# Optimization experiments

Measured on AMD Instinct MI355X. Metric: run time of the kernel, lower is better.

The kernel has to match this reference:

```python
import jax, jax.numpy as jnp
import numpy as np

N = 50000
E = 1600000
EP = 500000
D_IN, D_EMB = 64, 32


def setup_inputs() -> dict:
    key = jax.random.key(0)
    ks = jax.random.split(key, 12)
    return {
        "x": jax.random.normal(ks[0], (N, D_IN), dtype=jnp.float32),
        "W1": jax.random.normal(ks[1], (D_IN, D_EMB), dtype=jnp.float32) * (1.0 / np.sqrt(D_IN)),
        "b1": jnp.zeros((D_EMB,), dtype=jnp.float32),
        "W2": jax.random.normal(ks[2], (D_EMB, 2 * D_EMB), dtype=jnp.float32) * (1.0 / np.sqrt(D_EMB)),
        "b2": jnp.zeros((2 * D_EMB,), dtype=jnp.float32),
        "eps": jax.random.normal(ks[3], (N, D_EMB), dtype=jnp.float32),
        "edge_src": jax.random.randint(ks[4], (E,), 0, N, dtype=jnp.int32),
        "edge_dst": jax.random.randint(ks[5], (E,), 0, N, dtype=jnp.int32),
        "pos_src": jax.random.randint(ks[6], (EP,), 0, N, dtype=jnp.int32),
        "pos_dst": jax.random.randint(ks[7], (EP,), 0, N, dtype=jnp.int32),
        "neg_src": jax.random.randint(ks[8], (EP,), 0, N, dtype=jnp.int32),
        "neg_dst": jax.random.randint(ks[9], (EP,), 0, N, dtype=jnp.int32),
    }


def _degree_norms(src, dst, n):
    ones = jnp.ones(src.shape, dtype=jnp.float32)
    out_deg = jax.ops.segment_sum(ones, src, num_segments=n)
    in_deg = jax.ops.segment_sum(ones, dst, num_segments=n)
    # DGL GraphConv norm='both': clamp degrees to >=1, pow(-0.5)
    return jnp.clip(out_deg, 1.0) ** -0.5, jnp.clip(in_deg, 1.0) ** -0.5


def _graph_conv(h, src, dst, norm_src, norm_dst, W, b, n):
    # rst = D_dst^{-1/2} A D_src^{-1/2} h W + b
    msg = (h * norm_src[:, None])[src]                       # [E, d] gather
    agg = jax.ops.segment_sum(msg, dst, num_segments=n)      # [N, d] scatter-add
    return (agg * norm_dst[:, None]) @ W + b


def _dot_predict(z, u, v):
    # u_dot_v: per-edge inner product of endpoint embeddings
    return jnp.sum(z[u] * z[v], axis=-1)


def reference(x, W1, b1, W2, b2, eps, edge_src, edge_dst,
              pos_src, pos_dst, neg_src, neg_dst):
    n = x.shape[0]
    ns, nd = _degree_norms(edge_src, edge_dst, n)
    h = _graph_conv(x, edge_src, edge_dst, ns, nd, W1, b1, n)
    h = jax.nn.relu(h)  # dropout = identity (eval mode)
    h = _graph_conv(h, edge_src, edge_dst, ns, nd, W2, b2, n)
    mu, log_var = jnp.split(h, 2, axis=-1)
    sigma = jnp.exp(log_var / 2.0)
    z = mu + sigma * eps
    pos = _dot_predict(z, pos_src, pos_dst)
    neg = _dot_predict(z, neg_src, neg_dst)
    return pos, neg, mu, sigma
```

## Files before the change

kernel.cpp:

```cpp
#include <hip/hip_runtime.h>
#include <math.h>

#define NN  50000
#define NE  1600000
#define NEP 500000
#define DIN 64
#define DE  32

#define BKT_SH 7
#define NB     391
#define S1B    250
#define CHK    6400
#define HB     128
#define HCHK   12500
#define HWRD   12500
#define XWB    3125

__device__ __forceinline__ unsigned f2b(float f) {
    unsigned u = __float_as_uint(f);
    return (u + 0x7FFFu + ((u >> 16) & 1u)) >> 16;
}
__device__ __forceinline__ unsigned pack2(float a, float b) {
    return f2b(a) | (f2b(b) << 16);
}
__device__ __forceinline__ float blo(unsigned u) { return __uint_as_float(u << 16); }
__device__ __forceinline__ float bhi(unsigned u) { return __uint_as_float(u & 0xFFFF0000u); }

__global__ __launch_bounds__(256) void k_h1s1(const int* __restrict__ src,
                                              const int* __restrict__ dst,
                                              unsigned* __restrict__ partial,
                                              int* __restrict__ T) {
    __shared__ unsigned h[HWRD];
    int t = threadIdx.x;
    if (blockIdx.x < HB) {
        for (int i = t; i < HWRD; i += 256) h[i] = 0;
        __syncthreads();
        int beg = blockIdx.x * HCHK;
        for (int i = beg + t; i < beg + HCHK; i += 256) {
            int s = src[i];
            atomicAdd(&h[s >> 2], 1u << ((s & 3) * 8));
        }
        __syncthreads();
        unsigned* p = partial + (size_t)blockIdx.x * HWRD;
        for (int i = t; i < HWRD; i += 256) p[i] = h[i];
    } else {
        int b = blockIdx.x - HB;
        int* cd = (int*)h;
        for (int i = t; i < NB; i += 256) cd[i] = 0;
        __syncthreads();
        int beg = b * CHK;
        for (int i = beg + t; i < beg + CHK; i += 256)
            atomicAdd(&cd[dst[i] >> BKT_SH], 1);
        __syncthreads();
        for (int i = t; i < NB; i += 256) T[b * NB + i] = cd[i];
    }
}

__global__ __launch_bounds__(512) void k_s2h(const int* __restrict__ T,
                                             int* __restrict__ Base,
                                             int* __restrict__ BS,
                                             const unsigned* __restrict__ partial,
                                             int* __restrict__ degs) {
    int t = threadIdx.x;
    if (blockIdx.x == 0) {
        __shared__ int tot[512];
        int run = 0;
        if (t < NB) {
            for (int b = 0; b < S1B; b++) {
                Base[b * NB + t] = run;
                run += T[b * NB + t];
            }
        }
        tot[t] = (t < NB) ? run : 0;
        __syncthreads();
        for (int off = 1; off < 512; off <<= 1) {
            int v = (t >= off) ? tot[t - off] : 0;
            __syncthreads();
            tot[t] += v;
            __syncthreads();
        }
        if (t < NB) BS[t] = (t == 0) ? 0 : tot[t - 1];
        if (t == 0) BS[NB] = NE;
    } else {
        int w = (blockIdx.x - 1) * 512 + t;
        if (w < HWRD) {
            int c0 = 0, c1 = 0, c2 = 0, c3 = 0;
            for (int b = 0; b < HB; b++) {
                unsigned v = partial[(size_t)b * HWRD + w];
                c0 += (int)(v & 0xFFu);
                c1 += (int)((v >> 8) & 0xFFu);
                c2 += (int)((v >> 16) & 0xFFu);
                c3 += (int)(v >> 24);
            }
            ((int4*)degs)[w] = make_int4(c0, c1, c2, c3);
        }
    }
}

__global__ __launch_bounds__(512) void k_s3(const int* __restrict__ src,
                                            const int* __restrict__ dst,
                                            const int* __restrict__ T,
                                            const int* __restrict__ Base,
                                            const int* __restrict__ BS,
                                            unsigned* __restrict__ tmp) {
    __shared__ int scn[512];
    __shared__ int delta[NB];
    __shared__ int cur[NB];
    __shared__ unsigned buf[CHK];
    int t = threadIdx.x;
    int beg = blockIdx.x * CHK;
    scn[t] = (t < NB) ? T[blockIdx.x * NB + t] : 0;
    __syncthreads();
    for (int off = 1; off < 512; off <<= 1) {
        int v = (t >= off) ? scn[t - off] : 0;
        __syncthreads();
        scn[t] += v;
        __syncthreads();
    }
    if (t < NB) {
        int ls = (t == 0) ? 0 : scn[t - 1];
        cur[t] = ls;
        delta[t] = Base[blockIdx.x * NB + t] + BS[t] - ls;
    }
    __syncthreads();
    for (int i = t; i < CHK; i += 512) {
        int d = dst[beg + i];
        int s = src[beg + i];
        int lp = atomicAdd(&cur[d >> BKT_SH], 1);
        buf[lp] = (unsigned)s | ((unsigned)d << 16);
    }
    __syncthreads();
    for (int i = t; i < CHK; i += 512) {
        unsigned e = buf[i];
        tmp[delta[e >> (16 + BKT_SH)] + i] = e;
    }
}

__global__ __launch_bounds__(256) void k_s4x(const unsigned* __restrict__ tmp,
                                             const int* __restrict__ BS,
                                             int* __restrict__ csr,
                                             int* __restrict__ rowptr,
                                             const float* __restrict__ x,
                                             const float* __restrict__ W1,
                                             const int* __restrict__ degs,
                                             unsigned* __restrict__ xw1b) {
    __shared__ float sW[DIN * DE];
    int t = threadIdx.x;
    if (blockIdx.x < NB) {
        int* cnt = (int*)sW;
        int* scn = cnt + 128;
        int* cur = cnt + 256;
        int p = blockIdx.x;
        int ebeg = BS[p], eend = BS[p + 1];
        int ne = eend - ebeg;
        if (t < 128) cnt[t] = 0;
        __syncthreads();
        for (int i = t; i < ne; i += 256)
            atomicAdd(&cnt[(tmp[ebeg + i] >> 16) & 127], 1);
        __syncthreads();
        if (t < 128) scn[t] = cnt[t];
        __syncthreads();
        for (int off = 1; off < 128; off <<= 1) {
            int v = 0;
            if (t < 128 && t >= off) v = scn[t - off];
            __syncthreads();
            if (t < 128) scn[t] += v;
            __syncthreads();
        }
        if (t < 128) {
            int ex = (t == 0) ? 0 : scn[t - 1];
            cur[t] = ex;
            int node = (p << BKT_SH) + t;
            if (node < NN) rowptr[node] = ebeg + ex;
        }
        if (p == NB - 1 && t == 0) rowptr[NN] = NE;
        __syncthreads();
        for (int i = t; i < ne; i += 256) {
            unsigned e = tmp[ebeg + i];
            int lp = atomicAdd(&cur[(e >> 16) & 127], 1);
            csr[ebeg + lp] = (int)(e & 0xFFFFu);
        }
    } else {
        for (int i = t; i < DIN * DE; i += 256) sW[i] = W1[i];
        __syncthreads();
        int r  = (blockIdx.x - NB) * 16 + (t >> 4);
        int tc = t & 15;
        const float* xr = x + (size_t)r * DIN;
        float a0 = 0.f, a1 = 0.f;
#pragma unroll
        for (int k = 0; k < DIN; k++) {
            float v = xr[k];
            a0 += v * sW[k * DE + 2 * tc];
            a1 += v * sW[k * DE + 2 * tc + 1];
        }
        float ns = rsqrtf(fmaxf((float)degs[r], 1.0f));
        xw1b[r * 16 + tc] = pack2(a0 * ns, a1 * ns);
    }
}

__device__ __forceinline__ void acc8(float* a, uint4 w) {
    a[0] += blo(w.x); a[1] += bhi(w.x);
    a[2] += blo(w.y); a[3] += bhi(w.y);
    a[4] += blo(w.z); a[5] += bhi(w.z);
    a[6] += blo(w.w); a[7] += bhi(w.w);
}

__device__ __forceinline__ void gather_row(const int* __restrict__ csr,
                                           const uint4* __restrict__ msg,
                                           int beg, int end, int l, float* a) {
    int idx = beg;
    for (; idx + 8 <= end; idx += 8) {
        int s0 = csr[idx],     s1 = csr[idx + 1], s2 = csr[idx + 2], s3 = csr[idx + 3];
        int s4 = csr[idx + 4], s5 = csr[idx + 5], s6 = csr[idx + 6], s7 = csr[idx + 7];
        uint4 w0 = msg[s0 * 4 + l];
        uint4 w1 = msg[s1 * 4 + l];
        uint4 w2 = msg[s2 * 4 + l];
        uint4 w3 = msg[s3 * 4 + l];
        uint4 w4 = msg[s4 * 4 + l];
        uint4 w5 = msg[s5 * 4 + l];
        uint4 w6 = msg[s6 * 4 + l];
        uint4 w7 = msg[s7 * 4 + l];
        acc8(a, w0); acc8(a, w1); acc8(a, w2); acc8(a, w3);
        acc8(a, w4); acc8(a, w5); acc8(a, w6); acc8(a, w7);
    }
    for (; idx + 4 <= end; idx += 4) {
        int s0 = csr[idx], s1 = csr[idx + 1], s2 = csr[idx + 2], s3 = csr[idx + 3];
        uint4 w0 = msg[s0 * 4 + l];
        uint4 w1 = msg[s1 * 4 + l];
        uint4 w2 = msg[s2 * 4 + l];
        uint4 w3 = msg[s3 * 4 + l];
        acc8(a, w0); acc8(a, w1); acc8(a, w2); acc8(a, w3);
    }
    for (; idx < end; idx++) {
        uint4 w = msg[csr[idx] * 4 + l];
        acc8(a, w);
    }
}

__global__ __launch_bounds__(256) void k_g1(const int* __restrict__ rowptr,
                                            const int* __restrict__ csr,
                                            const uint4* __restrict__ msg,
                                            const int* __restrict__ degs,
                                            const float* __restrict__ b1,
                                            uint4* __restrict__ out) {
    int t = blockIdx.x * 256 + threadIdx.x;
    int r = t >> 2;
    int l = t & 3;
    if (r >= NN) return;
    int beg = rowptr[r];
    int end = rowptr[r + 1];
    float a[8] = {0, 0, 0, 0, 0, 0, 0, 0};
    gather_row(csr, msg, beg, end, l, a);
    float scd = rsqrtf(fmaxf((float)(end - beg), 1.0f));
    float scs = rsqrtf(fmaxf((float)degs[r], 1.0f));
    const float4* b14 = (const float4*)b1;
    float4 bb0 = b14[2 * l], bb1 = b14[2 * l + 1];
    float o0 = fmaxf(scd * a[0] + bb0.x, 0.f) * scs;
    float o1 = fmaxf(scd * a[1] + bb0.y, 0.f) * scs;
    float o2 = fmaxf(scd * a[2] + bb0.z, 0.f) * scs;
    float o3 = fmaxf(scd * a[3] + bb0.w, 0.f) * scs;
    float o4 = fmaxf(scd * a[4] + bb1.x, 0.f) * scs;
    float o5 = fmaxf(scd * a[5] + bb1.y, 0.f) * scs;
    float o6 = fmaxf(scd * a[6] + bb1.z, 0.f) * scs;
    float o7 = fmaxf(scd * a[7] + bb1.w, 0.f) * scs;
    out[r * 4 + l] = make_uint4(pack2(o0, o1), pack2(o2, o3), pack2(o4, o5), pack2(o6, o7));
}

__global__ __launch_bounds__(256) void k_g2f(const int* __restrict__ rowptr,
                                             const int* __restrict__ csr,
                                             const uint4* __restrict__ msg,
                                             const float* __restrict__ W2,
                                             const float* __restrict__ b2,
                                             const float* __restrict__ eps,
                                             float* __restrict__ mu,
                                             float* __restrict__ sigma,
                                             unsigned* __restrict__ zb) {
    __shared__ float sW[DE * 64];
    __shared__ float sb[64];
    int t = threadIdx.x;
    for (int i = t; i < DE * 64; i += 256) sW[i] = W2[i];
    if (t < 64) sb[t] = b2[t];
    __syncthreads();
    int g = blockIdx.x * 256 + t;
    int r = g >> 2;
    int l = g & 3;
    if (r >= NN) return;
    int beg = rowptr[r];
    int end = rowptr[r + 1];
    float a[8] = {0, 0, 0, 0, 0, 0, 0, 0};
    gather_row(csr, msg, beg, end, l, a);
    float scd = rsqrtf(fmaxf((float)(end - beg), 1.0f));
#pragma unroll
    for (int k = 0; k < 8; k++) a[k] *= scd;
    int cbase = 16 * l;
    float o3[16];
#pragma unroll
    for (int j = 0; j < 16; j++) o3[j] = sb[cbase + j];
#pragma unroll
    for (int d = 0; d < 4; d++) {
        int kb = 8 * (l ^ d);
#pragma unroll
        for (int k = 0; k < 8; k++) {
            float av = (d == 0) ? a[k] : __shfl_xor(a[k], d);
            const float* wrow = sW + (kb + k) * 64 + cbase;
#pragma unroll
            for (int j = 0; j < 16; j++) o3[j] += av * wrow[j];
        }
    }
    if (l < 2) {
        float4* mp = (float4*)(mu + (size_t)r * DE + 16 * l);
        mp[0] = make_float4(o3[0],  o3[1],  o3[2],  o3[3]);
        mp[1] = make_float4(o3[4],  o3[5],  o3[6],  o3[7]);
        mp[2] = make_float4(o3[8],  o3[9],  o3[10], o3[11]);
        mp[3] = make_float4(o3[12], o3[13], o3[14], o3[15]);
    }
    float muv[16];
#pragma unroll
    for (int j = 0; j < 16; j++) muv[j] = __shfl_xor(o3[j], 2);
    if (l >= 2) {
        int cc = 16 * (l - 2);
        const float4* ep = (const float4*)(eps + (size_t)r * DE + cc);
        float4 e0 = ep[0], e1 = ep[1], e2 = ep[2], e3 = ep[3];
        float ev[16] = {e0.x, e0.y, e0.z, e0.w, e1.x, e1.y, e1.z, e1.w,
                        e2.x, e2.y, e2.z, e2.w, e3.x, e3.y, e3.z, e3.w};
        float sgv[16], zv[16];
#pragma unroll
        for (int j = 0; j < 16; j++) {
            sgv[j] = expf(0.5f * o3[j]);
            zv[j]  = muv[j] + sgv[j] * ev[j];
        }
        float4* sp = (float4*)(sigma + (size_t)r * DE + cc);
        sp[0] = make_float4(sgv[0],  sgv[1],  sgv[2],  sgv[3]);
        sp[1] = make_float4(sgv[4],  sgv[5],  sgv[6],  sgv[7]);
        sp[2] = make_float4(sgv[8],  sgv[9],  sgv[10], sgv[11]);
        sp[3] = make_float4(sgv[12], sgv[13], sgv[14], sgv[15]);
        uint4* zp = (uint4*)(zb + (size_t)r * 16 + (l - 2) * 8);
        zp[0] = make_uint4(pack2(zv[0], zv[1]), pack2(zv[2], zv[3]),
                           pack2(zv[4], zv[5]), pack2(zv[6], zv[7]));
        zp[1] = make_uint4(pack2(zv[8],  zv[9]),  pack2(zv[10], zv[11]),
                           pack2(zv[12], zv[13]), pack2(zv[14], zv[15]));
    }
}

__global__ __launch_bounds__(256) void k_dot2(const uint4* __restrict__ zb4,
                                              const int* __restrict__ pu,
                                              const int* __restrict__ pv,
                                              const int* __restrict__ nu,
                                              const int* __restrict__ nv,
                                              float* __restrict__ out) {
    int t = blockIdx.x * 256 + threadIdx.x;
    int e = t >> 2;
    int l = t & 3;
    if (e < 2 * NEP) {
        int ee = (e < NEP) ? e : e - NEP;
        const int* uu = (e < NEP) ? pu : nu;
        const int* vv = (e < NEP) ? pv : nv;
        int a = uu[ee];
        int b = vv[ee];
        uint4 za = zb4[a * 4 + l];
        uint4 zc = zb4[b * 4 + l];
        float s = blo(za.x) * blo(zc.x) + bhi(za.x) * bhi(zc.x)
                + blo(za.y) * blo(zc.y) + bhi(za.y) * bhi(zc.y)
                + blo(za.z) * blo(zc.z) + bhi(za.z) * bhi(zc.z)
                + blo(za.w) * blo(zc.w) + bhi(za.w) * bhi(zc.w);
        s += __shfl_xor(s, 1);
        s += __shfl_xor(s, 2);
        if (l == 0) out[e] = s;
    }
}

extern "C" void kernel_launch(void* const* d_in, const int* in_sizes, int n_in,
                              void* d_out, int out_size, void* d_ws, size_t ws_size,
                              hipStream_t stream) {
    const float* x    = (const float*)d_in[0];
    const float* W1   = (const float*)d_in[1];
    const float* b1   = (const float*)d_in[2];
    const float* W2   = (const float*)d_in[3];
    const float* b2   = (const float*)d_in[4];
    const float* eps  = (const float*)d_in[5];
    const int*   esrc = (const int*)d_in[6];
    const int*   edst = (const int*)d_in[7];
    const int*   psrc = (const int*)d_in[8];
    const int*   pdst = (const int*)d_in[9];
    const int*   gsrc = (const int*)d_in[10];
    const int*   gdst = (const int*)d_in[11];

    float* out = (float*)d_out;
    float* pos = out;
    float* mu  = out + 2 * NEP;
    float* sg  = out + 2 * NEP + NN * DE;

    int* wi = (int*)d_ws;
    int*      rowptr  = wi;
    int*      T       = wi + 50001;
    int*      Base    = wi + 147751;
    int*      BS      = wi + 245501;
    int*      degs    = wi + 245896;
    int*      csr     = wi + 295896;
    unsigned* partial = (unsigned*)(wi + 1895896);
    unsigned* tmp     = (unsigned*)(wi + 3495896);
    unsigned* P0      = (unsigned*)(wi + 5095896);
    unsigned* P1      = P0 + 16 * NN;

    k_h1s1<<<HB + S1B, 256, 0, stream>>>(esrc, edst, partial, T);
    k_s2h <<<1 + (HWRD + 511) / 512, 512, 0, stream>>>(T, Base, BS, partial, degs);
    k_s3  <<<S1B, 512, 0, stream>>>(esrc, edst, T, Base, BS, tmp);
    k_s4x <<<NB + XWB, 256, 0, stream>>>(tmp, BS, csr, rowptr, x, W1, degs, P0);
    k_g1  <<<(NN * 4 + 255) / 256, 256, 0, stream>>>(rowptr, csr, (const uint4*)P0, degs, b1, (uint4*)P1);
    k_g2f <<<(NN * 4 + 255) / 256, 256, 0, stream>>>(rowptr, csr, (const uint4*)P1, W2, b2, eps, mu, sg, P0);
    k_dot2<<<(2 * NEP * 4) / 256, 256, 0, stream>>>((const uint4*)P0, psrc, pdst, gsrc, gdst, pos);
}
```

Baseline: 221.1 us.

## Split row gathers across two half-warps, halve histogram blocks, add nontemporal accesses

Each destination row in both aggregation kernels now uses 8 lanes instead of 4. The edge list is split in halves and the two partial sums are combined with a shuffle. The fused second-layer kernel now spreads its output columns over all 8 lanes, 8 columns each. The degree histogram runs in 64 blocks over larger chunks, so fewer per-block partial histograms have to be reduced. Several streaming loads and stores become nontemporal. The aim is more memory-level parallelism in the gathers and less reduction traffic, at the cost of extra lanes and shuffles per row and fewer histogram blocks in flight.

```diff
diff --git a/kernel.cpp b/kernel.cpp
--- a/kernel.cpp
+++ b/kernel.cpp
@@ -11,10 +11,12 @@
 #define NB     391
 #define S1B    250
 #define CHK    6400
-#define HB     128
-#define HCHK   12500
+#define HB     64
+#define HCHK   25000
 #define HWRD   12500
 #define XWB    3125
+
+typedef float f4 __attribute__((ext_vector_type(4)));
 
 __device__ __forceinline__ unsigned f2b(float f) {
     unsigned u = __float_as_uint(f);
@@ -42,7 +44,8 @@
         }
         __syncthreads();
         unsigned* p = partial + (size_t)blockIdx.x * HWRD;
-        for (int i = t; i < HWRD; i += 256) p[i] = h[i];
+        for (int i = t; i < HWRD; i += 256)
+            __builtin_nontemporal_store(h[i], p + i);
     } else {
         int b = blockIdx.x - HB;
         int* cd = (int*)h;
@@ -86,7 +89,7 @@
         if (w < HWRD) {
             int c0 = 0, c1 = 0, c2 = 0, c3 = 0;
             for (int b = 0; b < HB; b++) {
-                unsigned v = partial[(size_t)b * HWRD + w];
+                unsigned v = __builtin_nontemporal_load(partial + (size_t)b * HWRD + w);
                 c0 += (int)(v & 0xFFu);
                 c1 += (int)((v >> 8) & 0xFFu);
                 c2 += (int)((v >> 16) & 0xFFu);
@@ -244,13 +247,18 @@
                                             const float* __restrict__ b1,
                                             uint4* __restrict__ out) {
     int t = blockIdx.x * 256 + threadIdx.x;
-    int r = t >> 2;
+    int r = t >> 3;
     int l = t & 3;
+    int h = (t >> 2) & 1;
     if (r >= NN) return;
     int beg = rowptr[r];
     int end = rowptr[r + 1];
+    int mid = beg + ((end - beg) >> 1);
     float a[8] = {0, 0, 0, 0, 0, 0, 0, 0};
-    gather_row(csr, msg, beg, end, l, a);
+    gather_row(csr, msg, h ? mid : beg, h ? end : mid, l, a);
+#pragma unroll
+    for (int k = 0; k < 8; k++) a[k] += __shfl_xor(a[k], 4);
+    if (h) return;
     float scd = rsqrtf(fmaxf((float)(end - beg), 1.0f));
     float scs = rsqrtf(fmaxf((float)degs[r], 1.0f));
     const float4* b14 = (const float4*)b1;
@@ -282,20 +290,25 @@
     if (t < 64) sb[t] = b2[t];
     __syncthreads();
     int g = blockIdx.x * 256 + t;
-    int r = g >> 2;
+    int r = g >> 3;
     int l = g & 3;
+    int j = g & 7;
+    int h = (g >> 2) & 1;
     if (r >= NN) return;
     int beg = rowptr[r];
     int end = rowptr[r + 1];
+    int mid = beg + ((end - beg) >> 1);
     float a[8] = {0, 0, 0, 0, 0, 0, 0, 0};
-    gather_row(csr, msg, beg, end, l, a);
+    gather_row(csr, msg, h ? mid : beg, h ? end : mid, l, a);
+#pragma unroll
+    for (int k = 0; k < 8; k++) a[k] += __shfl_xor(a[k], 4);
     float scd = rsqrtf(fmaxf((float)(end - beg), 1.0f));
 #pragma unroll
     for (int k = 0; k < 8; k++) a[k] *= scd;
-    int cbase = 16 * l;
-    float o3[16];
-#pragma unroll
-    for (int j = 0; j < 16; j++) o3[j] = sb[cbase + j];
+    int cbase = 8 * j;
+    float o3[8];
+#pragma unroll
+    for (int c = 0; c < 8; c++) o3[c] = sb[cbase + c];
 #pragma unroll
     for (int d = 0; d < 4; d++) {
         int kb = 8 * (l ^ d);
@@ -304,41 +317,39 @@
             float av = (d == 0) ? a[k] : __shfl_xor(a[k], d);
             const float* wrow = sW + (kb + k) * 64 + cbase;
 #pragma unroll
-            for (int j = 0; j < 16; j++) o3[j] += av * wrow[j];
-        }
-    }
-    if (l < 2) {
-        float4* mp = (float4*)(mu + (size_t)r * DE + 16 * l);
-        mp[0] = make_float4(o3[0],  o3[1],  o3[2],  o3[3]);
-        mp[1] = make_float4(o3[4],  o3[5],  o3[6],  o3[7]);
-        mp[2] = make_float4(o3[8],  o3[9],  o3[10], o3[11]);
-        mp[3] = make_float4(o3[12], o3[13], o3[14], o3[15]);
-    }
-    float muv[16];
-#pragma unroll
-    for (int j = 0; j < 16; j++) muv[j] = __shfl_xor(o3[j], 2);
-    if (l >= 2) {
-        int cc = 16 * (l - 2);
-        const float4* ep = (const float4*)(eps + (size_t)r * DE + cc);
-        float4 e0 = ep[0], e1 = ep[1], e2 = ep[2], e3 = ep[3];
-        float ev[16] = {e0.x, e0.y, e0.z, e0.w, e1.x, e1.y, e1.z, e1.w,
-                        e2.x, e2.y, e2.z, e2.w, e3.x, e3.y, e3.z, e3.w};
-        float sgv[16], zv[16];
-#pragma unroll
-        for (int j = 0; j < 16; j++) {
-            sgv[j] = expf(0.5f * o3[j]);
-            zv[j]  = muv[j] + sgv[j] * ev[j];
-        }
-        float4* sp = (float4*)(sigma + (size_t)r * DE + cc);
-        sp[0] = make_float4(sgv[0],  sgv[1],  sgv[2],  sgv[3]);
-        sp[1] = make_float4(sgv[4],  sgv[5],  sgv[6],  sgv[7]);
-        sp[2] = make_float4(sgv[8],  sgv[9],  sgv[10], sgv[11]);
-        sp[3] = make_float4(sgv[12], sgv[13], sgv[14], sgv[15]);
-        uint4* zp = (uint4*)(zb + (size_t)r * 16 + (l - 2) * 8);
+            for (int c = 0; c < 8; c++) o3[c] += av * wrow[c];
+        }
+    }
+    if (j < 4) {
+        f4* mp = (f4*)(mu + (size_t)r * DE + cbase);
+        f4 m0 = {o3[0], o3[1], o3[2], o3[3]};
+        f4 m1 = {o3[4], o3[5], o3[6], o3[7]};
+        __builtin_nontemporal_store(m0, mp);
+        __builtin_nontemporal_store(m1, mp + 1);
+    }
+    float muv[8];
+#pragma unroll
+    for (int c = 0; c < 8; c++) muv[c] = __shfl_xor(o3[c], 4);
+    if (j >= 4) {
+        int cc = cbase - DE;
+        const f4* ep = (const f4*)(eps + (size_t)r * DE + cc);
+        f4 e0 = __builtin_nontemporal_load(ep);
+        f4 e1 = __builtin_nontemporal_load(ep + 1);
+        float ev[8] = {e0.x, e0.y, e0.z, e0.w, e1.x, e1.y, e1.z, e1.w};
+        float sgv[8], zv[8];
+#pragma unroll
+        for (int c = 0; c < 8; c++) {
+            sgv[c] = expf(0.5f * o3[c]);
+            zv[c]  = muv[c] + sgv[c] * ev[c];
+        }
+        f4* sp = (f4*)(sigma + (size_t)r * DE + cc);
+        f4 s0 = {sgv[0], sgv[1], sgv[2], sgv[3]};
+        f4 s1 = {sgv[4], sgv[5], sgv[6], sgv[7]};
+        __builtin_nontemporal_store(s0, sp);
+        __builtin_nontemporal_store(s1, sp + 1);
+        uint4* zp = (uint4*)(zb + (size_t)r * 16 + (j - 4) * 4);
         zp[0] = make_uint4(pack2(zv[0], zv[1]), pack2(zv[2], zv[3]),
                            pack2(zv[4], zv[5]), pack2(zv[6], zv[7]));
-        zp[1] = make_uint4(pack2(zv[8],  zv[9]),  pack2(zv[10], zv[11]),
-                           pack2(zv[12], zv[13]), pack2(zv[14], zv[15]));
     }
 }
 
@@ -355,8 +366,8 @@
         int ee = (e < NEP) ? e : e - NEP;
         const int* uu = (e < NEP) ? pu : nu;
         const int* vv = (e < NEP) ? pv : nv;
-        int a = uu[ee];
-        int b = vv[ee];
+        int a = __builtin_nontemporal_load(uu + ee);
+        int b = __builtin_nontemporal_load(vv + ee);
         uint4 za = zb4[a * 4 + l];
         uint4 zc = zb4[b * 4 + l];
         float s = blo(za.x) * blo(zc.x) + bhi(za.x) * bhi(zc.x)
@@ -365,7 +376,7 @@
                 + blo(za.w) * blo(zc.w) + bhi(za.w) * bhi(zc.w);
         s += __shfl_xor(s, 1);
         s += __shfl_xor(s, 2);
-        if (l == 0) out[e] = s;
+        if (l == 0) __builtin_nontemporal_store(s, out + e);
     }
 }
 
@@ -406,7 +417,7 @@
     k_s2h <<<1 + (HWRD + 511) / 512, 512, 0, stream>>>(T, Base, BS, partial, degs);
     k_s3  <<<S1B, 512, 0, stream>>>(esrc, edst, T, Base, BS, tmp);
     k_s4x <<<NB + XWB, 256, 0, stream>>>(tmp, BS, csr, rowptr, x, W1, degs, P0);
-    k_g1  <<<(NN * 4 + 255) / 256, 256, 0, stream>>>(rowptr, csr, (const uint4*)P0, degs, b1, (uint4*)P1);
-    k_g2f <<<(NN * 4 + 255) / 256, 256, 0, stream>>>(rowptr, csr, (const uint4*)P1, W2, b2, eps, mu, sg, P0);
+    k_g1  <<<(NN * 8 + 255) / 256, 256, 0, stream>>>(rowptr, csr, (const uint4*)P0, degs, b1, (uint4*)P1);
+    k_g2f <<<(NN * 8 + 255) / 256, 256, 0, stream>>>(rowptr, csr, (const uint4*)P1, W2, b2, eps, mu, sg, P0);
     k_dot2<<<(2 * NEP * 4) / 256, 256, 0, stream>>>((const uint4*)P0, psrc, pdst, gsrc, gdst, pos);
 }
```

After: 239.9 us. +8.5%, slower.
